# Optimization experiments

Hardware: AMD Instinct MI355X
Metric: run time of the kernel (lower is better)

Reference implementation:

```python
import jax, jax.numpy as jnp
import numpy as np

TOTAL = 131072   # total frames across all utterances
SEG = 256        # number of utterances
FEAT = 78        # input feature dim (hardcoded by Linear(78,1024))
HID = 1024
NCLS = 10


def _linear_params(key, fan_in, fan_out):
    # torch nn.Linear default init: U(-1/sqrt(fan_in), 1/sqrt(fan_in))
    bound = 1.0 / np.sqrt(fan_in)
    kw, kb = jax.random.split(key)
    W = jax.random.uniform(kw, (fan_in, fan_out), minval=-bound, maxval=bound, dtype=jnp.float32)
    b = jax.random.uniform(kb, (fan_out,), minval=-bound, maxval=bound, dtype=jnp.float32)
    return W, b


def setup_inputs() -> dict:
    key = jax.random.key(0)
    ks = jax.random.split(key, 8)
    # ragged lengths summing exactly to TOTAL
    rng = np.random.default_rng(0)
    raw = rng.integers(256, 768, size=SEG).astype(np.float64)
    lens = np.maximum(1, (raw * TOTAL / raw.sum()).astype(np.int64))
    lens[-1] += TOTAL - lens.sum()
    lengths = jnp.asarray(lens, dtype=jnp.int32)

    x = jax.random.normal(ks[0], (TOTAL, FEAT), dtype=jnp.float32)
    W1, b1 = _linear_params(ks[1], FEAT, HID)
    W2, b2 = _linear_params(ks[2], HID, HID)
    W3, b3 = _linear_params(ks[3], HID, HID)
    W4, b4 = _linear_params(ks[4], HID, HID)
    W5, b5 = _linear_params(ks[5], HID, 1)
    W6, b6 = _linear_params(ks[6], HID, HID)
    W7, b7 = _linear_params(ks[7], HID, NCLS)
    return dict(x=x, W1=W1, b1=b1, W2=W2, b2=b2, W3=W3, b3=b3, W4=W4, b4=b4,
                W5=W5, b5=b5, W6=W6, b6=b6, W7=W7, b7=b7, lengths=lengths)


def reference(x, W1, b1, W2, b2, W3, b3, W4, b4, W5, b5, W6, b6, W7, b7, lengths):
    h = jax.nn.relu(x @ W1 + b1)
    h = jax.nn.relu(h @ W2 + b2)
    h = jax.nn.relu(h @ W3 + b3)
    h = jax.nn.relu(h @ W4 + b4)            # [N, HID]
    scores = jax.nn.relu(h @ W5 + b5)[:, 0]  # per-frame attention logit [N]

    # per-segment softmax over frames, then weighted sum pooling (fused segment ops)
    n_seg = lengths.shape[0]
    seg = jnp.repeat(jnp.arange(n_seg, dtype=jnp.int32), lengths,
                     total_repeat_length=h.shape[0])          # [N] segment ids
    m = jax.ops.segment_max(scores, seg, num_segments=n_seg)  # stable softmax max
    e = jnp.exp(scores - m[seg])
    denom = jax.ops.segment_sum(e, seg, num_segments=n_seg)
    w = e / denom[seg]                                        # [N] softmax weights
    pooled = jax.ops.segment_sum(h * w[:, None], seg, num_segments=n_seg)  # [SEG, HID]

    out = jax.nn.relu(pooled @ W6 + b6) @ W7 + b7             # [SEG, 10]
    return out
```

## Files before the change

kernel.cpp:

```cpp
#include <hip/hip_runtime.h>
#include <hip/hip_fp16.h>

#define TOTAL 131072
#define SEGN  256
#define FEAT  78
#define FPAD  96
#define HID   1024
#define NCLS  10
#define FCHUNK 32

typedef __attribute__((ext_vector_type(8))) short short8;
typedef __attribute__((ext_vector_type(4))) float floatx4;

typedef __attribute__((address_space(1))) void gvoid_t;
typedef __attribute__((address_space(3))) void svoid_t;

__device__ __forceinline__ void async_copy16(const void* gsrc, void* ldst) {
    __builtin_amdgcn_global_load_lds((gvoid_t*)(void*)gsrc, (svoid_t*)ldst, 16, 0, 0);
}

__device__ __forceinline__ int xswz(int r) { return (r & 3) ^ ((r >> 2) & 3); }


__global__ void conv_x_slab(const float* __restrict__ x, __half* __restrict__ xb,
                            int row0, int rows) {
    int idx = blockIdx.x * 256 + threadIdx.x;
    if (idx >= rows * FPAD) return;
    int col = idx % FPAD;
    int r   = idx / FPAD;
    float v = (col < FEAT) ? x[(size_t)(row0 + r) * FEAT + col] : 0.0f;
    xb[idx] = __float2half(v);
}

__global__ void conv_wt_kernel(const float* __restrict__ W, __half* __restrict__ Wt,
                               int K, int N, int Kpad) {
    int idx = blockIdx.x * 256 + threadIdx.x;
    if (idx >= N * Kpad) return;
    int k = idx % Kpad;
    int n = idx / Kpad;
    float v = (k < K) ? W[(size_t)k * N + n] : 0.0f;
    Wt[idx] = __float2half(v);
}

__global__ void conv_w4_kernel(const float* __restrict__ W2, const float* __restrict__ W3,
                               const float* __restrict__ W4, const float* __restrict__ W6,
                               __half* __restrict__ w2t, __half* __restrict__ w3t,
                               __half* __restrict__ w4t, __half* __restrict__ w6t) {
    int idx = blockIdx.x * 256 + threadIdx.x;
    if (idx >= HID * HID) return;
    int k = idx % HID;
    int n = idx / HID;
    const float* Ws[4] = {W2, W3, W4, W6};
    __half* Ts[4] = {w2t, w3t, w4t, w6t};
    int w = blockIdx.y;
    Ts[w][idx] = __float2half(Ws[w][(size_t)k * HID + n]);
}


__global__ __launch_bounds__(256, 2)
void gemm_f16(const __half* __restrict__ A, const __half* __restrict__ Bt,
              __half* __restrict__ C, const float* __restrict__ bias,
              int M, int N, int K, int relu_flag)
{
    __shared__ __align__(16) short smem[128 * 32 * 2];
    short* lds_a = smem;
    short* lds_b = smem + 128 * 32;

    const int t   = threadIdx.x;
    const int nbn = N >> 7;
    const int nbm = M >> 7;
    int bm, bn;
    {
        const int b = blockIdx.x;
        if ((nbm & 7) == 0) {
            const int xcd = b & 7;
            const int j   = b >> 3;
            bm = xcd * (nbm >> 3) + j / nbn;
            bn = j % nbn;
        } else {
            bn = b % nbn;
            bm = b / nbn;
        }
    }
    const size_t m0 = (size_t)bm * 128;
    const size_t n0 = (size_t)bn * 128;
    const int wave = t >> 6, lane = t & 63;
    const int wm = (wave >> 1) << 6;
    const int wn = (wave & 1) << 6;
    const int l16 = lane & 15, q = lane >> 4;

    floatx4 acc[4][4] = {};

    const int c0 = t, c1 = t + 256;
    const int r0s = c0 >> 2, r1s = c1 >> 2;
    const int g0 = (c0 & 3) ^ xswz(r0s);
    const int g1 = (c1 & 3) ^ xswz(r1s);
    const __half* a0 = A  + (m0 + (size_t)r0s) * K + g0 * 8;
    const __half* a1 = A  + (m0 + (size_t)r1s) * K + g1 * 8;
    const __half* b0 = Bt + (n0 + (size_t)r0s) * K + g0 * 8;
    const __half* b1 = Bt + (n0 + (size_t)r1s) * K + g1 * 8;
    short* la0 = &lds_a[c0 * 8];
    short* la1 = &lds_a[c1 * 8];
    short* lb0 = &lds_b[c0 * 8];
    short* lb1 = &lds_b[c1 * 8];

    const int xq = (q ^ (l16 & 3) ^ ((l16 >> 2) & 3)) * 8;

    for (int k0 = 0; k0 < K; k0 += 32) {
        __syncthreads();
        async_copy16(a0 + k0, la0);
        async_copy16(a1 + k0, la1);
        async_copy16(b0 + k0, lb0);
        async_copy16(b1 + k0, lb1);
        __syncthreads();

        short8 af[4], bf[4];
#pragma unroll
        for (int i = 0; i < 4; ++i)
            af[i] = *(const short8*)&lds_a[(wm + i * 16 + l16) * 32 + xq];
#pragma unroll
        for (int i = 0; i < 4; ++i)
            bf[i] = *(const short8*)&lds_b[(wn + i * 16 + l16) * 32 + xq];

#pragma unroll
        for (int mi = 0; mi < 4; ++mi)
#pragma unroll
            for (int ni = 0; ni < 4; ++ni)
                acc[mi][ni] = __builtin_amdgcn_mfma_f32_16x16x32_f16(
                    af[mi], bf[ni], acc[mi][ni], 0, 0, 0);
    }

    __half* ct = (__half*)smem;
#pragma unroll
    for (int h = 0; h < 2; ++h) {
        __syncthreads();
        if (wm == h * 64) {
#pragma unroll
            for (int ni = 0; ni < 4; ++ni) {
                const int col = wn + ni * 16 + l16;
                const float bv = bias[n0 + col];
#pragma unroll
                for (int mi = 0; mi < 4; ++mi) {
                    const int r0l = mi * 16 + q * 4;
#pragma unroll
                    for (int r = 0; r < 4; ++r) {
                        float v = acc[mi][ni][r] + bv;
                        if (relu_flag) v = fmaxf(v, 0.0f);
                        ct[(r0l + r) * 128 + col] = __float2half(v);
                    }
                }
            }
        }
        __syncthreads();
#pragma unroll
        for (int it = 0; it < 4; ++it) {
            const int chunk = it * 256 + t;
            const int row = chunk >> 4;
            const int off = (chunk & 15) * 8;
            *(short8*)&C[(m0 + h * 64 + row) * N + n0 + off] =
                *(const short8*)&ct[row * 128 + off];
        }
    }
}


__global__ __launch_bounds__(256, 2)
void gemm_k96(const __half* __restrict__ A, const __half* __restrict__ Bt,
              __half* __restrict__ C, const float* __restrict__ bias, int M, int N)
{
    __shared__ __align__(16) short smem[2 * 128 * 96];
    short* lds_a = smem;
    short* lds_b = smem + 128 * 96;

    const int t   = threadIdx.x;
    const int nbn = N >> 7;
    const int nbm = M >> 7;
    int bm, bn;
    {
        const int b = blockIdx.x;
        if ((nbm & 7) == 0) {
            const int xcd = b & 7;
            const int j   = b >> 3;
            bm = xcd * (nbm >> 3) + j / nbn;
            bn = j % nbn;
        } else {
            bn = b % nbn;
            bm = b / nbn;
        }
    }
    const size_t m0 = (size_t)bm * 128;
    const size_t n0 = (size_t)bn * 128;
    const int wave = t >> 6, lane = t & 63;
    const int wm = (wave >> 1) << 6;
    const int wn = (wave & 1) << 6;
    const int l16 = lane & 15, q = lane >> 4;

#pragma unroll
    for (int i = 0; i < 6; ++i) {
        const int c = i * 256 + t;
        const int r = c / 12, j = c % 12;
        const int g = (j >> 2) * 4 + ((j & 3) ^ xswz(r));
        async_copy16(A  + (m0 + (size_t)r) * 96 + g * 8, &lds_a[c * 8]);
        async_copy16(Bt + (n0 + (size_t)r) * 96 + g * 8, &lds_b[c * 8]);
    }
    __syncthreads();

    floatx4 acc[4][4] = {};
    const int xql = ((q ^ (l16 & 3) ^ ((l16 >> 2) & 3))) * 8;
#pragma unroll
    for (int ks = 0; ks < 3; ++ks) {
        short8 af[4], bf[4];
        const int xo = ks * 32 + xql;
#pragma unroll
        for (int i = 0; i < 4; ++i)
            af[i] = *(const short8*)&lds_a[(wm + i * 16 + l16) * 96 + xo];
#pragma unroll
        for (int i = 0; i < 4; ++i)
            bf[i] = *(const short8*)&lds_b[(wn + i * 16 + l16) * 96 + xo];
#pragma unroll
        for (int mi = 0; mi < 4; ++mi)
#pragma unroll
            for (int ni = 0; ni < 4; ++ni)
                acc[mi][ni] = __builtin_amdgcn_mfma_f32_16x16x32_f16(
                    af[mi], bf[ni], acc[mi][ni], 0, 0, 0);
    }

    __half* ct = (__half*)smem;
#pragma unroll
    for (int h = 0; h < 2; ++h) {
        __syncthreads();
        if (wm == h * 64) {
#pragma unroll
            for (int ni = 0; ni < 4; ++ni) {
                const int col = wn + ni * 16 + l16;
                const float bv = bias[n0 + col];
#pragma unroll
                for (int mi = 0; mi < 4; ++mi) {
                    const int r0l = mi * 16 + q * 4;
#pragma unroll
                    for (int r = 0; r < 4; ++r) {
                        float v = fmaxf(acc[mi][ni][r] + bv, 0.0f);
                        ct[(r0l + r) * 128 + col] = __float2half(v);
                    }
                }
            }
        }
        __syncthreads();
#pragma unroll
        for (int it = 0; it < 4; ++it) {
            const int chunk = it * 256 + t;
            const int row = chunk >> 4;
            const int off = (chunk & 15) * 8;
            *(short8*)&C[(m0 + h * 64 + row) * N + n0 + off] =
                *(const short8*)&ct[row * 128 + off];
        }
    }
}


__global__ void seg_offsets_kernel(const int* __restrict__ lengths, int* __restrict__ off) {
    if (blockIdx.x == 0 && threadIdx.x == 0) {
        int a = 0;
        off[0] = 0;
        for (int i = 0; i < SEGN; ++i) { a += lengths[i]; off[i + 1] = a; }
    }
}


__global__ __launch_bounds__(256)
void scorepool_kernel(const __half* __restrict__ h4, int slab_beg,
                      const float* __restrict__ W5, const float* __restrict__ b5,
                      const int* __restrict__ segoff,
                      float* __restrict__ pooled, float* __restrict__ denom)
{
    __shared__ float e_sh[FCHUNK];
    const int t = threadIdx.x, wave = t >> 6, lane = t & 63;
    const int f0 = slab_beg + blockIdx.x * FCHUNK;
    const float b5v = b5[0];

#pragma unroll
    for (int i = 0; i < 8; ++i) {
        const int fl = wave * 8 + i;
        const __half* row = h4 + (size_t)(f0 - slab_beg + fl) * HID + lane * 16;
        const float* wv = W5 + lane * 16;
        short8 r0 = *(const short8*)row;
        short8 r1 = *(const short8*)(row + 8);
        float s = 0.f;
#pragma unroll
        for (int j = 0; j < 8; ++j) s += __half2float(((const __half*)&r0)[j]) * wv[j];
#pragma unroll
        for (int j = 0; j < 8; ++j) s += __half2float(((const __half*)&r1)[j]) * wv[j + 8];
#pragma unroll
        for (int o = 32; o > 0; o >>= 1) s += __shfl_down(s, o);
        if (lane == 0)
            e_sh[fl] = __expf(fminf(fmaxf(s + b5v, 0.0f), 80.0f));
    }
    __syncthreads();

    const int c0 = t * 4;
    int lo = 0, hi = SEGN - 1;
    while (lo < hi) {
        int mid = (lo + hi + 1) >> 1;
        if (segoff[mid] <= f0) lo = mid; else hi = mid - 1;
    }
    int s = lo;
    int f = f0;
    const int fend = f0 + FCHUNK;
    const __half* base = h4 + (size_t)(f0 - slab_beg) * HID + c0;
    while (f < fend) {
        int send = segoff[s + 1];
        if (send > fend) send = fend;
        float a0 = 0.f, a1 = 0.f, a2 = 0.f, a3 = 0.f, es = 0.f;
        for (; f < send; ++f, base += HID) {
            float e = e_sh[f - f0];
            const __half2* r2 = (const __half2*)base;
            float2 u = __half22float2(r2[0]);
            float2 v = __half22float2(r2[1]);
            a0 += e * u.x; a1 += e * u.y; a2 += e * v.x; a3 += e * v.y;
            es += e;
        }
        float* p = pooled + (size_t)s * HID + c0;
        atomicAdd(p,     a0);
        atomicAdd(p + 1, a1);
        atomicAdd(p + 2, a2);
        atomicAdd(p + 3, a3);
        if (t == 0) atomicAdd(&denom[s], es);
        ++s;
    }
}


__global__ __launch_bounds__(256)
void finalize_pool_kernel(const float* __restrict__ pooled, const float* __restrict__ denom,
                          __half* __restrict__ poolh)
{
    int s = blockIdx.x, t = threadIdx.x;
    float inv = 1.0f / denom[s];
    for (int j = t; j < HID; j += 256)
        poolh[(size_t)s * HID + j] = __float2half(pooled[(size_t)s * HID + j] * inv);
}


__global__ void final_kernel(const __half* __restrict__ z, const float* __restrict__ W7,
                             const float* __restrict__ b7, float* __restrict__ out) {
    int s = blockIdx.x, t = threadIdx.x;
    float loc[NCLS];
#pragma unroll
    for (int c = 0; c < NCLS; ++c) loc[c] = 0.f;
    for (int k = t; k < HID; k += 256) {
        float zk = __half2float(z[(size_t)s * HID + k]);
        const float* wr = W7 + k * NCLS;
#pragma unroll
        for (int c = 0; c < NCLS; ++c) loc[c] += zk * wr[c];
    }
#pragma unroll
    for (int c = 0; c < NCLS; ++c)
#pragma unroll
        for (int o = 32; o > 0; o >>= 1) loc[c] += __shfl_down(loc[c], o);
    __shared__ float accs[NCLS];
    if (t < NCLS) accs[t] = 0.f;
    __syncthreads();
    if ((t & 63) == 0)
        for (int c = 0; c < NCLS; ++c) atomicAdd(&accs[c], loc[c]);
    __syncthreads();
    if (t < NCLS) out[s * NCLS + t] = accs[t] + b7[t];
}


extern "C" void kernel_launch(void* const* d_in, const int* in_sizes, int n_in,
                              void* d_out, int out_size, void* d_ws, size_t ws_size,
                              hipStream_t stream) {
    const float* x  = (const float*)d_in[0];
    const float* W1 = (const float*)d_in[1];
    const float* b1 = (const float*)d_in[2];
    const float* W2 = (const float*)d_in[3];
    const float* b2 = (const float*)d_in[4];
    const float* W3 = (const float*)d_in[5];
    const float* b3 = (const float*)d_in[6];
    const float* W4 = (const float*)d_in[7];
    const float* b4 = (const float*)d_in[8];
    const float* W5 = (const float*)d_in[9];
    const float* b5 = (const float*)d_in[10];
    const float* W6 = (const float*)d_in[11];
    const float* b6 = (const float*)d_in[12];
    const float* W7 = (const float*)d_in[13];
    const float* b7 = (const float*)d_in[14];
    const int* lengths = (const int*)d_in[15];
    float* out = (float*)d_out;

    char* ws = (char*)d_ws;
    size_t off = 0;
    auto take = [&](size_t bytes) -> char* {
        char* p = ws + off;
        off = (off + bytes + 255) & ~(size_t)255;
        return p;
    };
    __half* w1t   = (__half*)take((size_t)HID * FPAD * 2);
    __half* w2t   = (__half*)take((size_t)HID * HID * 2);
    __half* w3t   = (__half*)take((size_t)HID * HID * 2);
    __half* w4t   = (__half*)take((size_t)HID * HID * 2);
    __half* w6t   = (__half*)take((size_t)HID * HID * 2);
    int*    segoff = (int*)take((SEGN + 1) * 4);
    float*  pooled = (float*)take((size_t)SEGN * HID * 4);
    float*  denom  = (float*)take(SEGN * 4);
    __half* poolh  = (__half*)take((size_t)SEGN * HID * 2);
    __half* z      = (__half*)take((size_t)SEGN * HID * 2);

    int R = TOTAL;
    while (R > 1024) {
        size_t need = off + (size_t)R * FPAD * 2 + 2 * (size_t)R * HID * 2 + 3 * 256;
        if (need <= ws_size) break;
        R >>= 1;
    }
    __half* slabX = (__half*)take((size_t)R * FPAD * 2);
    __half* slabA = (__half*)take((size_t)R * HID * 2);
    __half* slabB = (__half*)take((size_t)R * HID * 2);

    seg_offsets_kernel<<<1, 64, 0, stream>>>(lengths, segoff);
    hipMemsetAsync(pooled, 0, (size_t)SEGN * HID * 4, stream);
    hipMemsetAsync(denom, 0, SEGN * 4, stream);

    conv_wt_kernel<<<(HID * FPAD + 255) / 256, 256, 0, stream>>>(W1, w1t, FEAT, HID, FPAD);
    dim3 gW((HID * HID + 255) / 256, 4);
    conv_w4_kernel<<<gW, 256, 0, stream>>>(W2, W3, W4, W6, w2t, w3t, w4t, w6t);

    const int nBlocksSlab = (R / 128) * (HID / 128);
    for (int sb = 0; sb < TOTAL; sb += R) {
        conv_x_slab<<<(R * FPAD + 255) / 256, 256, 0, stream>>>(x, slabX, sb, R);
        gemm_k96<<<nBlocksSlab, 256, 0, stream>>>(slabX, w1t, slabA, b1, R, HID);
        gemm_f16<<<nBlocksSlab, 256, 0, stream>>>(slabA, w2t, slabB, b2, R, HID, HID, 1);
        gemm_f16<<<nBlocksSlab, 256, 0, stream>>>(slabB, w3t, slabA, b3, R, HID, HID, 1);
        gemm_f16<<<nBlocksSlab, 256, 0, stream>>>(slabA, w4t, slabB, b4, R, HID, HID, 1);
        scorepool_kernel<<<R / FCHUNK, 256, 0, stream>>>(slabB, sb, W5, b5, segoff, pooled, denom);
    }

    finalize_pool_kernel<<<SEGN, 256, 0, stream>>>(pooled, denom, poolh);
    const int nBlocksHead = (SEGN / 128) * (HID / 128);
    gemm_f16<<<nBlocksHead, 256, 0, stream>>>(poolh, w6t, z, b6, SEGN, HID, HID, 1);
    final_kernel<<<SEGN, 256, 0, stream>>>(z, W7, b7, out);
}
```

Before: 1.369 ms.

## Double K-step per barrier and drop LDS XOR swizzle in GEMM kernels

The main f16 GEMM now loads two 32-wide K slices per iteration into two separate LDS buffers, halving the number of barrier pairs per tile. The XOR swizzle on LDS layout is removed from both GEMM kernels, so addresses use plain row-major offsets. This lowers barrier and address-arithmetic overhead but doubles LDS use, which may hurt occupancy, and the unswizzled layout may bring back LDS bank conflicts on fragment reads.

```diff
diff --git a/kernel.cpp b/kernel.cpp
--- a/kernel.cpp
+++ b/kernel.cpp
@@ -18,8 +18,6 @@
 __device__ __forceinline__ void async_copy16(const void* gsrc, void* ldst) {
     __builtin_amdgcn_global_load_lds((gvoid_t*)(void*)gsrc, (svoid_t*)ldst, 16, 0, 0);
 }
-
-__device__ __forceinline__ int xswz(int r) { return (r & 3) ^ ((r >> 2) & 3); }
 
 
 __global__ void conv_x_slab(const float* __restrict__ x, __half* __restrict__ xb,
@@ -62,9 +60,11 @@
               __half* __restrict__ C, const float* __restrict__ bias,
               int M, int N, int K, int relu_flag)
 {
-    __shared__ __align__(16) short smem[128 * 32 * 2];
-    short* lds_a = smem;
-    short* lds_b = smem + 128 * 32;
+    __shared__ __align__(16) short smem[4 * 128 * 32];
+    short* lds_a0 = smem;
+    short* lds_a1 = smem + 128 * 32;
+    short* lds_b0 = smem + 2 * 128 * 32;
+    short* lds_b1 = smem + 3 * 128 * 32;
 
     const int t   = threadIdx.x;
     const int nbn = N >> 7;
@@ -92,36 +92,51 @@
     floatx4 acc[4][4] = {};
 
     const int c0 = t, c1 = t + 256;
-    const int r0s = c0 >> 2, r1s = c1 >> 2;
-    const int g0 = (c0 & 3) ^ xswz(r0s);
-    const int g1 = (c1 & 3) ^ xswz(r1s);
-    const __half* a0 = A  + (m0 + (size_t)r0s) * K + g0 * 8;
-    const __half* a1 = A  + (m0 + (size_t)r1s) * K + g1 * 8;
-    const __half* b0 = Bt + (n0 + (size_t)r0s) * K + g0 * 8;
-    const __half* b1 = Bt + (n0 + (size_t)r1s) * K + g1 * 8;
-    short* la0 = &lds_a[c0 * 8];
-    short* la1 = &lds_a[c1 * 8];
-    short* lb0 = &lds_b[c0 * 8];
-    short* lb1 = &lds_b[c1 * 8];
-
-    const int xq = (q ^ (l16 & 3) ^ ((l16 >> 2) & 3)) * 8;
-
-    for (int k0 = 0; k0 < K; k0 += 32) {
-        __syncthreads();
-        async_copy16(a0 + k0, la0);
-        async_copy16(a1 + k0, la1);
-        async_copy16(b0 + k0, lb0);
-        async_copy16(b1 + k0, lb1);
+    const __half* a0 = A  + (m0 + (size_t)(c0 >> 2)) * K + (c0 & 3) * 8;
+    const __half* a1 = A  + (m0 + (size_t)(c1 >> 2)) * K + (c1 & 3) * 8;
+    const __half* b0 = Bt + (n0 + (size_t)(c0 >> 2)) * K + (c0 & 3) * 8;
+    const __half* b1 = Bt + (n0 + (size_t)(c1 >> 2)) * K + (c1 & 3) * 8;
+    short* lA0_0 = &lds_a0[c0 * 8];
+    short* lA0_1 = &lds_a0[c1 * 8];
+    short* lA1_0 = &lds_a1[c0 * 8];
+    short* lA1_1 = &lds_a1[c1 * 8];
+    short* lB0_0 = &lds_b0[c0 * 8];
+    short* lB0_1 = &lds_b0[c1 * 8];
+    short* lB1_0 = &lds_b1[c0 * 8];
+    short* lB1_1 = &lds_b1[c1 * 8];
+
+    for (int k0 = 0; k0 < K; k0 += 64) {
+        __syncthreads();
+        async_copy16(a0 + k0, lA0_0);
+        async_copy16(a1 + k0, lA0_1);
+        async_copy16(b0 + k0, lB0_0);
+        async_copy16(b1 + k0, lB0_1);
+        async_copy16(a0 + k0 + 32, lA1_0);
+        async_copy16(a1 + k0 + 32, lA1_1);
+        async_copy16(b0 + k0 + 32, lB1_0);
+        async_copy16(b1 + k0 + 32, lB1_1);
         __syncthreads();
 
         short8 af[4], bf[4];
 #pragma unroll
         for (int i = 0; i < 4; ++i)
-            af[i] = *(const short8*)&lds_a[(wm + i * 16 + l16) * 32 + xq];
-#pragma unroll
-        for (int i = 0; i < 4; ++i)
-            bf[i] = *(const short8*)&lds_b[(wn + i * 16 + l16) * 32 + xq];
-
+            af[i] = *(const short8*)&lds_a0[(wm + i * 16 + l16) * 32 + q * 8];
+#pragma unroll
+        for (int i = 0; i < 4; ++i)
+            bf[i] = *(const short8*)&lds_b0[(wn + i * 16 + l16) * 32 + q * 8];
+#pragma unroll
+        for (int mi = 0; mi < 4; ++mi)
+#pragma unroll
+            for (int ni = 0; ni < 4; ++ni)
+                acc[mi][ni] = __builtin_amdgcn_mfma_f32_16x16x32_f16(
+                    af[mi], bf[ni], acc[mi][ni], 0, 0, 0);
+
+#pragma unroll
+        for (int i = 0; i < 4; ++i)
+            af[i] = *(const short8*)&lds_a1[(wm + i * 16 + l16) * 32 + q * 8];
+#pragma unroll
+        for (int i = 0; i < 4; ++i)
+            bf[i] = *(const short8*)&lds_b1[(wn + i * 16 + l16) * 32 + q * 8];
 #pragma unroll
         for (int mi = 0; mi < 4; ++mi)
 #pragma unroll
@@ -199,18 +214,16 @@
     for (int i = 0; i < 6; ++i) {
         const int c = i * 256 + t;
         const int r = c / 12, j = c % 12;
-        const int g = (j >> 2) * 4 + ((j & 3) ^ xswz(r));
-        async_copy16(A  + (m0 + (size_t)r) * 96 + g * 8, &lds_a[c * 8]);
-        async_copy16(Bt + (n0 + (size_t)r) * 96 + g * 8, &lds_b[c * 8]);
+        async_copy16(A  + (m0 + (size_t)r) * 96 + j * 8, &lds_a[c * 8]);
+        async_copy16(Bt + (n0 + (size_t)r) * 96 + j * 8, &lds_b[c * 8]);
     }
     __syncthreads();
 
     floatx4 acc[4][4] = {};
-    const int xql = ((q ^ (l16 & 3) ^ ((l16 >> 2) & 3))) * 8;
 #pragma unroll
     for (int ks = 0; ks < 3; ++ks) {
         short8 af[4], bf[4];
-        const int xo = ks * 32 + xql;
+        const int xo = ks * 32 + q * 8;
 #pragma unroll
         for (int i = 0; i < 4; ++i)
             af[i] = *(const short8*)&lds_a[(wm + i * 16 + l16) * 96 + xo];
```

Result: faster. 1.330 ms (-2.9%).
